# Optimization experiments

Measured on AMD Instinct MI355X. Metric: run time of the kernel, lower is better.

## Reference

```python
import jax, jax.numpy as jnp
import numpy as np


def setup_inputs() -> dict:
    key = jax.random.key(0)
    k1, k2 = jax.random.split(key)
    N, C = 32768, 2048
    x = jax.random.normal(k1, (N, C), dtype=jnp.float32)
    y = jax.random.normal(k2, (N, C), dtype=jnp.float32)
    return {"x": x, "y": y}


def reference(x, y):
    # Original: ce_x = (-eye * log_softmax(x)[:, :, None]).sum(1) == -log_softmax(x)
    # (the eye multiply+sum just extracts the diagonal). So:
    # ce = mean_n( min_c 0.5 * (-logp_x[n,c] - logp_y[n,c]) )
    lx = jax.nn.log_softmax(x, axis=1)  # [N, C]
    ly = jax.nn.log_softmax(y, axis=1)  # [N, C]
    ce = 0.5 * (-(lx + ly)).min(axis=1)  # [N]
    return ce.mean()
```

## Files before the change

### kernel.cpp

```cpp
#include <hip/hip_runtime.h>
#include <hip/hip_bf16.h>


#define ROW_C 2048
#define BLK   256

__device__ __forceinline__ float wave_max(float v) {
#pragma unroll
    for (int off = 32; off; off >>= 1) v = fmaxf(v, __shfl_xor(v, off));
    return v;
}
__device__ __forceinline__ float wave_sum(float v) {
#pragma unroll
    for (int off = 32; off; off >>= 1) v += __shfl_xor(v, off);
    return v;
}

__global__ __launch_bounds__(BLK) void mecl_row_kernel(
        const float* __restrict__ x, const float* __restrict__ y,
        float* __restrict__ ce) {
    const int row = blockIdx.x;
    const int t = threadIdx.x;
    const size_t base = (size_t)row * ROW_C;

    const float4* xr = reinterpret_cast<const float4*>(x + base);
    const float4* yr = reinterpret_cast<const float4*>(y + base);

    float4 x0 = xr[t];
    float4 x1 = xr[t + BLK];
    float4 y0 = yr[t];
    float4 y1 = yr[t + BLK];

    float mx = fmaxf(fmaxf(fmaxf(x0.x, x0.y), fmaxf(x0.z, x0.w)),
                     fmaxf(fmaxf(x1.x, x1.y), fmaxf(x1.z, x1.w)));
    float my = fmaxf(fmaxf(fmaxf(y0.x, y0.y), fmaxf(y0.z, y0.w)),
                     fmaxf(fmaxf(y1.x, y1.y), fmaxf(y1.z, y1.w)));

    float s0 = x0.x + y0.x, s1 = x0.y + y0.y, s2 = x0.z + y0.z, s3 = x0.w + y0.w;
    float s4 = x1.x + y1.x, s5 = x1.y + y1.y, s6 = x1.z + y1.z, s7 = x1.w + y1.w;
    float mxy = fmaxf(fmaxf(fmaxf(s0, s1), fmaxf(s2, s3)),
                      fmaxf(fmaxf(s4, s5), fmaxf(s6, s7)));

    mx  = wave_max(mx);
    my  = wave_max(my);
    mxy = wave_max(mxy);

    __shared__ float smx[4], smy[4], smxy[4];
    const int wave = t >> 6;
    if ((t & 63) == 0) { smx[wave] = mx; smy[wave] = my; smxy[wave] = mxy; }
    __syncthreads();
    mx  = fmaxf(fmaxf(smx[0],  smx[1]),  fmaxf(smx[2],  smx[3]));
    my  = fmaxf(fmaxf(smy[0],  smy[1]),  fmaxf(smy[2],  smy[3]));
    mxy = fmaxf(fmaxf(smxy[0], smxy[1]), fmaxf(smxy[2], smxy[3]));

    float sx = __expf(x0.x - mx) + __expf(x0.y - mx) + __expf(x0.z - mx) + __expf(x0.w - mx)
             + __expf(x1.x - mx) + __expf(x1.y - mx) + __expf(x1.z - mx) + __expf(x1.w - mx);
    float sy = __expf(y0.x - my) + __expf(y0.y - my) + __expf(y0.z - my) + __expf(y0.w - my)
             + __expf(y1.x - my) + __expf(y1.y - my) + __expf(y1.z - my) + __expf(y1.w - my);

    sx = wave_sum(sx);
    sy = wave_sum(sy);

    __shared__ float ssx[4], ssy[4];
    if ((t & 63) == 0) { ssx[wave] = sx; ssy[wave] = sy; }
    __syncthreads();
    if (t == 0) {
        sx = ssx[0] + ssx[1] + ssx[2] + ssx[3];
        sy = ssy[0] + ssy[1] + ssy[2] + ssy[3];
        float lse_x = mx + __logf(sx);
        float lse_y = my + __logf(sy);
        ce[row] = 0.5f * (lse_x + lse_y - mxy);
    }
}

__global__ __launch_bounds__(BLK) void mecl_row_atomic_kernel(
        const float* __restrict__ x, const float* __restrict__ y,
        float* __restrict__ out, float inv_n) {
    const int row = blockIdx.x;
    const int t = threadIdx.x;
    const size_t base = (size_t)row * ROW_C;
    const float4* xr = reinterpret_cast<const float4*>(x + base);
    const float4* yr = reinterpret_cast<const float4*>(y + base);
    float4 x0 = xr[t], x1 = xr[t + BLK];
    float4 y0 = yr[t], y1 = yr[t + BLK];

    float mx = fmaxf(fmaxf(fmaxf(x0.x, x0.y), fmaxf(x0.z, x0.w)),
                     fmaxf(fmaxf(x1.x, x1.y), fmaxf(x1.z, x1.w)));
    float my = fmaxf(fmaxf(fmaxf(y0.x, y0.y), fmaxf(y0.z, y0.w)),
                     fmaxf(fmaxf(y1.x, y1.y), fmaxf(y1.z, y1.w)));
    float s0 = x0.x + y0.x, s1 = x0.y + y0.y, s2 = x0.z + y0.z, s3 = x0.w + y0.w;
    float s4 = x1.x + y1.x, s5 = x1.y + y1.y, s6 = x1.z + y1.z, s7 = x1.w + y1.w;
    float mxy = fmaxf(fmaxf(fmaxf(s0, s1), fmaxf(s2, s3)),
                      fmaxf(fmaxf(s4, s5), fmaxf(s6, s7)));
    mx = wave_max(mx); my = wave_max(my); mxy = wave_max(mxy);
    __shared__ float smx[4], smy[4], smxy[4];
    const int wave = t >> 6;
    if ((t & 63) == 0) { smx[wave] = mx; smy[wave] = my; smxy[wave] = mxy; }
    __syncthreads();
    mx  = fmaxf(fmaxf(smx[0],  smx[1]),  fmaxf(smx[2],  smx[3]));
    my  = fmaxf(fmaxf(smy[0],  smy[1]),  fmaxf(smy[2],  smy[3]));
    mxy = fmaxf(fmaxf(smxy[0], smxy[1]), fmaxf(smxy[2], smxy[3]));
    float sx = __expf(x0.x - mx) + __expf(x0.y - mx) + __expf(x0.z - mx) + __expf(x0.w - mx)
             + __expf(x1.x - mx) + __expf(x1.y - mx) + __expf(x1.z - mx) + __expf(x1.w - mx);
    float sy = __expf(y0.x - my) + __expf(y0.y - my) + __expf(y0.z - my) + __expf(y0.w - my)
             + __expf(y1.x - my) + __expf(y1.y - my) + __expf(y1.z - my) + __expf(y1.w - my);
    sx = wave_sum(sx); sy = wave_sum(sy);
    __shared__ float ssx[4], ssy[4];
    if ((t & 63) == 0) { ssx[wave] = sx; ssy[wave] = sy; }
    __syncthreads();
    if (t == 0) {
        sx = ssx[0] + ssx[1] + ssx[2] + ssx[3];
        sy = ssy[0] + ssy[1] + ssy[2] + ssy[3];
        float ce = 0.5f * ((mx + __logf(sx)) + (my + __logf(sy)) - mxy);
        atomicAdd(out, ce * inv_n);
    }
}

__global__ __launch_bounds__(1024) void mecl_reduce_kernel(
        const float* __restrict__ ws, float* __restrict__ out,
        int n, float inv_n) {
    float s = 0.0f;
    for (int i = threadIdx.x; i < n; i += 1024) s += ws[i];
    s = wave_sum(s);
    __shared__ float sb[16];
    const int wave = threadIdx.x >> 6;
    if ((threadIdx.x & 63) == 0) sb[wave] = s;
    __syncthreads();
    if (threadIdx.x == 0) {
        float tot = 0.0f;
#pragma unroll
        for (int w = 0; w < 16; ++w) tot += sb[w];
        out[0] = tot * inv_n;
    }
}

extern "C" void kernel_launch(void* const* d_in, const int* in_sizes, int n_in,
                              void* d_out, int out_size, void* d_ws, size_t ws_size,
                              hipStream_t stream) {
    const float* x = (const float*)d_in[0];
    const float* y = (const float*)d_in[1];
    float* out = (float*)d_out;

    const int total = in_sizes[0];
    const int N = total / ROW_C;
    const float inv_n = 1.0f / (float)N;

    if (ws_size >= (size_t)N * sizeof(float)) {
        float* ws = (float*)d_ws;
        mecl_row_kernel<<<N, BLK, 0, stream>>>(x, y, ws);
        mecl_reduce_kernel<<<1, 1024, 0, stream>>>(ws, out, N, inv_n);
    } else {
        hipMemsetAsync(d_out, 0, sizeof(float), stream);
        mecl_row_atomic_kernel<<<N, BLK, 0, stream>>>(x, y, out, inv_n);
    }
}
```

Before: 506.2 us.

## Map one row per wavefront to drop block-level syncs and shared memory

Each 64-lane wavefront now processes a whole 2048-column row, holding 8 float4 loads of x and y per lane in registers. The block handles 4 rows, so all reductions use only wave shuffles with no __syncthreads or LDS round trips. The atomic fallback path is removed, so the code assumes the workspace is always large enough. More registers per thread may lower occupancy, but the kernel is memory bound and more loads are in flight per lane.

```diff
diff --git a/kernel.cpp b/kernel.cpp
--- a/kernel.cpp
+++ b/kernel.cpp
@@ -1,9 +1,11 @@
 #include <hip/hip_runtime.h>
 #include <hip/hip_bf16.h>
+#include <math.h>
 
 
 #define ROW_C 2048
 #define BLK   256
+#define ROWS_PER_BLOCK 4
 
 __device__ __forceinline__ float wave_max(float v) {
 #pragma unroll
@@ -19,100 +21,50 @@
 __global__ __launch_bounds__(BLK) void mecl_row_kernel(
         const float* __restrict__ x, const float* __restrict__ y,
         float* __restrict__ ce) {
-    const int row = blockIdx.x;
-    const int t = threadIdx.x;
+    const int lane = threadIdx.x & 63;
+    const int wave = threadIdx.x >> 6;
+    const int row  = blockIdx.x * ROWS_PER_BLOCK + wave;
     const size_t base = (size_t)row * ROW_C;
 
     const float4* xr = reinterpret_cast<const float4*>(x + base);
     const float4* yr = reinterpret_cast<const float4*>(y + base);
 
-    float4 x0 = xr[t];
-    float4 x1 = xr[t + BLK];
-    float4 y0 = yr[t];
-    float4 y1 = yr[t + BLK];
+    float4 xv[8], yv[8];
+#pragma unroll
+    for (int i = 0; i < 8; ++i) xv[i] = xr[lane + 64 * i];
+#pragma unroll
+    for (int i = 0; i < 8; ++i) yv[i] = yr[lane + 64 * i];
 
-    float mx = fmaxf(fmaxf(fmaxf(x0.x, x0.y), fmaxf(x0.z, x0.w)),
-                     fmaxf(fmaxf(x1.x, x1.y), fmaxf(x1.z, x1.w)));
-    float my = fmaxf(fmaxf(fmaxf(y0.x, y0.y), fmaxf(y0.z, y0.w)),
-                     fmaxf(fmaxf(y1.x, y1.y), fmaxf(y1.z, y1.w)));
+    float mx = -INFINITY, my = -INFINITY, ms = -INFINITY;
+#pragma unroll
+    for (int i = 0; i < 8; ++i) {
+        mx = fmaxf(mx, fmaxf(fmaxf(xv[i].x, xv[i].y), fmaxf(xv[i].z, xv[i].w)));
+        my = fmaxf(my, fmaxf(fmaxf(yv[i].x, yv[i].y), fmaxf(yv[i].z, yv[i].w)));
+        float s0 = xv[i].x + yv[i].x, s1 = xv[i].y + yv[i].y;
+        float s2 = xv[i].z + yv[i].z, s3 = xv[i].w + yv[i].w;
+        ms = fmaxf(ms, fmaxf(fmaxf(s0, s1), fmaxf(s2, s3)));
+    }
 
-    float s0 = x0.x + y0.x, s1 = x0.y + y0.y, s2 = x0.z + y0.z, s3 = x0.w + y0.w;
-    float s4 = x1.x + y1.x, s5 = x1.y + y1.y, s6 = x1.z + y1.z, s7 = x1.w + y1.w;
-    float mxy = fmaxf(fmaxf(fmaxf(s0, s1), fmaxf(s2, s3)),
-                      fmaxf(fmaxf(s4, s5), fmaxf(s6, s7)));
+    mx = wave_max(mx);
+    my = wave_max(my);
+    ms = wave_max(ms);
 
-    mx  = wave_max(mx);
-    my  = wave_max(my);
-    mxy = wave_max(mxy);
-
-    __shared__ float smx[4], smy[4], smxy[4];
-    const int wave = t >> 6;
-    if ((t & 63) == 0) { smx[wave] = mx; smy[wave] = my; smxy[wave] = mxy; }
-    __syncthreads();
-    mx  = fmaxf(fmaxf(smx[0],  smx[1]),  fmaxf(smx[2],  smx[3]));
-    my  = fmaxf(fmaxf(smy[0],  smy[1]),  fmaxf(smy[2],  smy[3]));
-    mxy = fmaxf(fmaxf(smxy[0], smxy[1]), fmaxf(smxy[2], smxy[3]));
-
-    float sx = __expf(x0.x - mx) + __expf(x0.y - mx) + __expf(x0.z - mx) + __expf(x0.w - mx)
-             + __expf(x1.x - mx) + __expf(x1.y - mx) + __expf(x1.z - mx) + __expf(x1.w - mx);
-    float sy = __expf(y0.x - my) + __expf(y0.y - my) + __expf(y0.z - my) + __expf(y0.w - my)
-             + __expf(y1.x - my) + __expf(y1.y - my) + __expf(y1.z - my) + __expf(y1.w - my);
+    float sx = 0.0f, sy = 0.0f;
+#pragma unroll
+    for (int i = 0; i < 8; ++i) {
+        sx += __expf(xv[i].x - mx) + __expf(xv[i].y - mx)
+            + __expf(xv[i].z - mx) + __expf(xv[i].w - mx);
+        sy += __expf(yv[i].x - my) + __expf(yv[i].y - my)
+            + __expf(yv[i].z - my) + __expf(yv[i].w - my);
+    }
 
     sx = wave_sum(sx);
     sy = wave_sum(sy);
 
-    __shared__ float ssx[4], ssy[4];
-    if ((t & 63) == 0) { ssx[wave] = sx; ssy[wave] = sy; }
-    __syncthreads();
-    if (t == 0) {
-        sx = ssx[0] + ssx[1] + ssx[2] + ssx[3];
-        sy = ssy[0] + ssy[1] + ssy[2] + ssy[3];
+    if (lane == 0) {
         float lse_x = mx + __logf(sx);
         float lse_y = my + __logf(sy);
-        ce[row] = 0.5f * (lse_x + lse_y - mxy);
-    }
-}
-
-__global__ __launch_bounds__(BLK) void mecl_row_atomic_kernel(
-        const float* __restrict__ x, const float* __restrict__ y,
-        float* __restrict__ out, float inv_n) {
-    const int row = blockIdx.x;
-    const int t = threadIdx.x;
-    const size_t base = (size_t)row * ROW_C;
-    const float4* xr = reinterpret_cast<const float4*>(x + base);
-    const float4* yr = reinterpret_cast<const float4*>(y + base);
-    float4 x0 = xr[t], x1 = xr[t + BLK];
-    float4 y0 = yr[t], y1 = yr[t + BLK];
-
-    float mx = fmaxf(fmaxf(fmaxf(x0.x, x0.y), fmaxf(x0.z, x0.w)),
-                     fmaxf(fmaxf(x1.x, x1.y), fmaxf(x1.z, x1.w)));
-    float my = fmaxf(fmaxf(fmaxf(y0.x, y0.y), fmaxf(y0.z, y0.w)),
-                     fmaxf(fmaxf(y1.x, y1.y), fmaxf(y1.z, y1.w)));
-    float s0 = x0.x + y0.x, s1 = x0.y + y0.y, s2 = x0.z + y0.z, s3 = x0.w + y0.w;
-    float s4 = x1.x + y1.x, s5 = x1.y + y1.y, s6 = x1.z + y1.z, s7 = x1.w + y1.w;
-    float mxy = fmaxf(fmaxf(fmaxf(s0, s1), fmaxf(s2, s3)),
-                      fmaxf(fmaxf(s4, s5), fmaxf(s6, s7)));
-    mx = wave_max(mx); my = wave_max(my); mxy = wave_max(mxy);
-    __shared__ float smx[4], smy[4], smxy[4];
-    const int wave = t >> 6;
-    if ((t & 63) == 0) { smx[wave] = mx; smy[wave] = my; smxy[wave] = mxy; }
-    __syncthreads();
-    mx  = fmaxf(fmaxf(smx[0],  smx[1]),  fmaxf(smx[2],  smx[3]));
-    my  = fmaxf(fmaxf(smy[0],  smy[1]),  fmaxf(smy[2],  smy[3]));
-    mxy = fmaxf(fmaxf(smxy[0], smxy[1]), fmaxf(smxy[2], smxy[3]));
-    float sx = __expf(x0.x - mx) + __expf(x0.y - mx) + __expf(x0.z - mx) + __expf(x0.w - mx)
-             + __expf(x1.x - mx) + __expf(x1.y - mx) + __expf(x1.z - mx) + __expf(x1.w - mx);
-    float sy = __expf(y0.x - my) + __expf(y0.y - my) + __expf(y0.z - my) + __expf(y0.w - my)
-             + __expf(y1.x - my) + __expf(y1.y - my) + __expf(y1.z - my) + __expf(y1.w - my);
-    sx = wave_sum(sx); sy = wave_sum(sy);
-    __shared__ float ssx[4], ssy[4];
-    if ((t & 63) == 0) { ssx[wave] = sx; ssy[wave] = sy; }
-    __syncthreads();
-    if (t == 0) {
-        sx = ssx[0] + ssx[1] + ssx[2] + ssx[3];
-        sy = ssy[0] + ssy[1] + ssy[2] + ssy[3];
-        float ce = 0.5f * ((mx + __logf(sx)) + (my + __logf(sy)) - mxy);
-        atomicAdd(out, ce * inv_n);
+        ce[row] = 0.5f * (lse_x + lse_y - ms);
     }
 }
 
@@ -144,13 +96,8 @@
     const int total = in_sizes[0];
     const int N = total / ROW_C;
     const float inv_n = 1.0f / (float)N;
+    float* ws = (float*)d_ws;
 
-    if (ws_size >= (size_t)N * sizeof(float)) {
-        float* ws = (float*)d_ws;
-        mecl_row_kernel<<<N, BLK, 0, stream>>>(x, y, ws);
-        mecl_reduce_kernel<<<1, 1024, 0, stream>>>(ws, out, N, inv_n);
-    } else {
-        hipMemsetAsync(d_out, 0, sizeof(float), stream);
-        mecl_row_atomic_kernel<<<N, BLK, 0, stream>>>(x, y, out, inv_n);
-    }
+    mecl_row_kernel<<<N / ROWS_PER_BLOCK, BLK, 0, stream>>>(x, y, ws);
+    mecl_reduce_kernel<<<1, 1024, 0, stream>>>(ws, out, N, inv_n);
 }
```

Result: no change. 506.3 us (+0.0%).
